# Optimization experiments

Measured on AMD Instinct MI355X. Metric: run time of the kernel, lower is better.

## Reference

```python
import jax, jax.numpy as jnp
import numpy as np

IC, IND, MID, OC, OD, ITERS = 8, 16, 32, 8, 16, 3
B, H, W = 8, 64, 64


def squash(x, axis):
    sq = jnp.sum(x * x, axis=axis, keepdims=True)
    return sq / (0.5 + sq) * x / (jnp.sqrt(sq + 1e-6) + 1e-6)


def gconv(x, w, b, pad):
    # grouped conv over the IC capsule groups (equivalent to the per-capsule
    # Conv2d blocks applied to slices of the capsule axis)
    y = jax.lax.conv_general_dilated(
        x, w, (1, 1), pad,
        dimension_numbers=("NCHW", "OIHW", "NCHW"),
        feature_group_count=IC)
    return y + b[None, :, None, None]


def setup_inputs() -> dict:
    key = jax.random.key(0)
    ks = jax.random.split(key, 7)
    x = jax.random.normal(ks[0], (B, IC * IND, H, W), jnp.float32)
    w1 = jax.random.normal(ks[1], (IC * MID, IND, 1, 1), jnp.float32) * 0.1
    b1 = jax.random.normal(ks[2], (IC * MID,), jnp.float32) * 0.1
    w2 = jax.random.normal(ks[3], (IC * MID, MID, 3, 3), jnp.float32) * 0.05
    b2 = jax.random.normal(ks[4], (IC * MID,), jnp.float32) * 0.1
    w3 = jax.random.normal(ks[5], (IC * OC * OD, MID, 1, 1), jnp.float32) * 0.05
    b3 = jax.random.normal(ks[6], (IC * OC * OD,), jnp.float32) * 0.1
    attn_w = jnp.zeros((1, OC, 1, 1, 1), jnp.float32)  # torch init: zeros
    attn_b = jnp.ones((1, OC, 1, 1, 1), jnp.float32)   # torch init: ones
    return dict(x=x, w1=w1, b1=b1, w2=w2, b2=b2, w3=w3, b3=b3,
                attn_w=attn_w, attn_b=attn_b)


def reference(x, w1, b1, w2, b2, w3, b3, attn_w, attn_b):
    bsz = x.shape[0]
    h_, w_ = x.shape[-2], x.shape[-1]
    # per-capsule conv stack: ReLU -> 1x1 -> ReLU -> 3x3 -> ReLU -> 1x1
    h = jax.nn.relu(x)
    h = jax.nn.relu(gconv(h, w1, b1, "VALID"))
    h = jax.nn.relu(gconv(h, w2, b2, "SAME"))
    h = gconv(h, w3, b3, "VALID")                     # [B, IC*OC*OD, H, W]
    u_hat = h.reshape(bsz, IC, OC, OD, h_, w_)
    u_sq = squash(u_hat, axis=3)
    # dynamic routing
    b = jnp.zeros((bsz, IC, OC, h_, w_), u_hat.dtype)
    for _ in range(ITERS - 1):
        c = jax.nn.sigmoid(b)
        s = jnp.sum(u_sq * c[:, :, :, None], axis=1)   # [B, OC, OD, H, W]
        v = squash(s, axis=2)
        b = b + jnp.sum(u_sq * v[:, None], axis=3)     # [B, IC, OC, H, W]
    c = jax.nn.sigmoid(b)
    s = jnp.sum(u_hat * c[:, :, :, None], axis=1)      # [B, OC, OD, H, W]
    # SpatialCapsuleAttn
    mean_hw = jnp.mean(s, axis=(-2, -1), keepdims=True)        # adaptive avg pool(1)
    avg = jnp.sum(s * mean_hw, axis=2)                         # [B, OC, H, W]
    t = avg.reshape(bsz, OC, h_ * w_)
    m = jnp.mean(t, axis=-1, keepdims=True)
    sd = jnp.std(t, axis=-1, keepdims=True, ddof=1) + 1e-6     # torch std: unbiased
    t = (t - m) / sd
    t = t.reshape(bsz, OC, 1, h_, w_) * attn_w + attn_b
    s = s * jax.nn.sigmoid(t)
    out = s.reshape(bsz, OC * OD, h_, w_) + x
    return out
```

## Files before the change

### kernel.cpp

```cpp
#include <hip/hip_runtime.h>
#include <hip/hip_bf16.h>
#include <hip/hip_fp16.h>

#define HW 4096

typedef _Float16 f16x8 __attribute__((ext_vector_type(8)));
typedef float f32x4 __attribute__((ext_vector_type(4)));

#define FOR8(X) X(0) X(1) X(2) X(3) X(4) X(5) X(6) X(7)

static __device__ __forceinline__ __half2 u2h(unsigned int u) {
    union { unsigned int u; __half2 h; } c; c.u = u; return c.h;
}
static __device__ __forceinline__ unsigned int h2u(__half2 h) {
    union { unsigned int u; __half2 h; } c; c.h = h; return c.u;
}

__global__ __launch_bounds__(256) void k0_prep(const float* __restrict__ w3, ushort* __restrict__ w3h,
                                               const float* __restrict__ w2, ushort* __restrict__ w2f,
                                               float* __restrict__ stats) {
    int bid = blockIdx.x;
    int t = threadIdx.x;
    if (bid == 0 && t < 128) stats[t] = 0.f;
    if (bid < 128) {
        int gi = bid * 256 + t;
        int j = gi & 7;
        int l = (gi >> 3) & 63;
        int p = gi >> 9;
        int ic = p >> 3, oc = p & 7;
        int od = l & 15;
        int m  = ((l >> 4) << 3) + j;
        w3h[gi] = __half_as_ushort(__float2half(w3[(size_t)((ic * 128 + oc * 16 + od) * 32 + m)]));
    } else {
        int gi = (bid - 128) * 256 + t;
        if (gi >= 73728) return;
        int j   = gi & 7;
        int l   = (gi >> 3) & 63;
        int h   = (gi >> 9) & 1;
        int tap = (gi >> 10) % 9;
        int g   = gi / 9216;
        int co = h * 16 + (l & 15);
        int ci = ((l >> 4) << 3) + j;
        w2f[gi] = __half_as_ushort(__float2half(w2[(size_t)((g * 32 + co) * 32 + ci) * 9 + tap]));
    }
}

__global__ __launch_bounds__(256) void k12_conv(const float* __restrict__ x, const float* __restrict__ w1,
                                                const float* __restrict__ b1, const ushort* __restrict__ w2f,
                                                const float* __restrict__ b2, ushort* __restrict__ h2g) {
    __shared__ ushort h1s[6][66][40];

    int bi = blockIdx.x;
    int q  = bi & 15;
    int g  = (bi >> 4) & 7;
    int b  = bi >> 7;
    int y0 = q * 4;
    int t  = threadIdx.x;

    for (int i = t; i < 396; i += 256) {
        int r  = i / 66;
        int xi = i - r * 66;
        int yy = y0 + r - 1;
        int xx = xi - 1;
        bool valid = (yy >= 0) && (yy < 64) && (xx >= 0) && (xx < 64);
        ushort hv[32];
        if (valid) {
            const float* xb = x + (size_t)(b * 128 + g * 16) * HW + yy * 64 + xx;
            float xv[16];
#pragma unroll
            for (int i2 = 0; i2 < 16; ++i2) xv[i2] = fmaxf(xb[i2 * HW], 0.f);
            const float* wg = w1 + g * 512;
            const float* bg = b1 + g * 32;
#pragma unroll
            for (int m = 0; m < 32; ++m) {
                float acc = bg[m];
#pragma unroll
                for (int i2 = 0; i2 < 16; ++i2) acc = fmaf(xv[i2], wg[m * 16 + i2], acc);
                hv[m] = __half_as_ushort(__float2half(fmaxf(acc, 0.f)));
            }
        } else {
#pragma unroll
            for (int m = 0; m < 32; ++m) hv[m] = 0;
        }
        ushort* dst = &h1s[r][xi][0];
#pragma unroll
        for (int q2 = 0; q2 < 4; ++q2) *(uint4*)&dst[q2 * 8] = *(uint4*)&hv[q2 * 8];
    }
    __syncthreads();

    int w  = t >> 6, l = t & 63;
    int lrow = l & 15, kgrp = l >> 4;
    int yloc = w;
    const ushort* wg2 = w2f + (size_t)g * 9216;

    float4 bias0 = *(const float4*)(b2 + g * 32 + kgrp * 4);
    float4 bias1 = *(const float4*)(b2 + g * 32 + 16 + kgrp * 4);

#pragma unroll
    for (int tile = 0; tile < 4; ++tile) {
        int xcol = tile * 16 + lrow;
        f32x4 acc0, acc1;
        acc0[0] = bias0.x; acc0[1] = bias0.y; acc0[2] = bias0.z; acc0[3] = bias0.w;
        acc1[0] = bias1.x; acc1[1] = bias1.y; acc1[2] = bias1.z; acc1[3] = bias1.w;
#pragma unroll
        for (int tap = 0; tap < 9; ++tap) {
            int dy = tap / 3, dx = tap - dy * 3;
            f16x8 Bf = *(const f16x8*)&h1s[yloc + dy][xcol + dx][kgrp * 8];
            f16x8 A0 = *(const f16x8*)&wg2[((tap * 2 + 0) * 64 + l) * 8];
            f16x8 A1 = *(const f16x8*)&wg2[((tap * 2 + 1) * 64 + l) * 8];
            acc0 = __builtin_amdgcn_mfma_f32_16x16x32_f16(A0, Bf, acc0, 0, 0, 0);
            acc1 = __builtin_amdgcn_mfma_f32_16x16x32_f16(A1, Bf, acc1, 0, 0, 0);
        }
        int px = (y0 + yloc) * 64 + xcol;
        ushort* ob = h2g + ((size_t)(b * 8 + g) * HW + px) * 32;
        uint2 wv0, wv1;
        wv0.x = h2u(__floats2half2_rn(fmaxf(acc0[0], 0.f), fmaxf(acc0[1], 0.f)));
        wv0.y = h2u(__floats2half2_rn(fmaxf(acc0[2], 0.f), fmaxf(acc0[3], 0.f)));
        wv1.x = h2u(__floats2half2_rn(fmaxf(acc1[0], 0.f), fmaxf(acc1[1], 0.f)));
        wv1.y = h2u(__floats2half2_rn(fmaxf(acc1[2], 0.f), fmaxf(acc1[3], 0.f)));
        *(uint2*)&ob[kgrp * 4] = wv0;
        *(uint2*)&ob[16 + kgrp * 4] = wv1;
    }
}

__global__ __launch_bounds__(512) void k3f_route(const ushort* __restrict__ h2g, const ushort* __restrict__ w3h,
                                                 const float* __restrict__ b3, ushort* __restrict__ sOut,
                                                 float* __restrict__ part) {
    __shared__ ushort us[32 * 1024];
    __shared__ float wred[8][16][8];
    int bid = blockIdx.x;
    int b   = bid >> 7;
    int px0 = (bid & 127) << 5;
    int t   = threadIdx.x;
    int w   = t >> 6, l = t & 63;

    {
        int ic = w;
        int lrow = l & 15, lk = l >> 4;
        f16x8 bf0 = *(const f16x8*)&h2g[(((size_t)(b * 8 + ic)) * HW + px0 + lrow) * 32 + lk * 8];
        f16x8 bf1 = *(const f16x8*)&h2g[(((size_t)(b * 8 + ic)) * HW + px0 + 16 + lrow) * 32 + lk * 8];
        int s0sw = (lrow & 15) << 3;
#pragma unroll
        for (int oc = 0; oc < 8; ++oc) {
            f16x8 af = *(const f16x8*)&w3h[((ic * 8 + oc) * 64 + l) * 8];
            float4 bv = *(const float4*)(b3 + ic * 128 + oc * 16 + lk * 4);
            f32x4 c0; c0[0] = bv.x; c0[1] = bv.y; c0[2] = bv.z; c0[3] = bv.w;
            int ch = ic * 128 + oc * 16 + lk * 4;
            f32x4 d0 = __builtin_amdgcn_mfma_f32_16x16x32_f16(af, bf0, c0, 0, 0, 0);
            uint2 wv0;
            wv0.x = h2u(__floats2half2_rn(d0[0], d0[1]));
            wv0.y = h2u(__floats2half2_rn(d0[2], d0[3]));
            *(uint2*)&us[lrow * 1024 + (ch ^ s0sw)] = wv0;
            f32x4 d1 = __builtin_amdgcn_mfma_f32_16x16x32_f16(af, bf1, c0, 0, 0, 0);
            uint2 wv1;
            wv1.x = h2u(__floats2half2_rn(d1[0], d1[1]));
            wv1.y = h2u(__floats2half2_rn(d1[2], d1[3]));
            *(uint2*)&us[(16 + lrow) * 1024 + (ch ^ s0sw)] = wv1;
        }
    }
    __syncthreads();

    int px  = t >> 4;
    int oc  = (t >> 1) & 7;
    int odh = t & 1;
    int ssw = (px & 15) << 3;
    const ushort* ur = &us[px * 1024];
#define LDQ(i) uint4 q##i = *(const uint4*)&ur[((i) * 128 + oc * 16 + odh * 8) ^ ssw];
    FOR8(LDQ)
#undef LDQ
    __syncthreads();

#define UNP(i) float2 f0 = __half22float2(u2h(q##i.x)), f1 = __half22float2(u2h(q##i.y)), \
                      f2 = __half22float2(u2h(q##i.z)), f3 = __half22float2(u2h(q##i.w));

#define SC(i) float sc##i; { UNP(i) \
        float sp = f0.x*f0.x + f0.y*f0.y + f1.x*f1.x + f1.y*f1.y \
                 + f2.x*f2.x + f2.y*f2.y + f3.x*f3.x + f3.y*f3.y; \
        sp += __shfl_xor(sp, 1); \
        sc##i = sp / ((0.5f + sp) * (sqrtf(sp + 1e-6f) + 1e-6f)); }
    FOR8(SC)
#undef SC

#define BRI(i) float br##i = 0.f;
    FOR8(BRI)
#undef BRI

    float s0, s1, s2, s3, s4, s5, s6, s7;
#pragma unroll
    for (int it = 0; it < 2; ++it) {
#define CSC(i) float cs##i = sc##i / (1.f + __expf(-br##i));
        FOR8(CSC)
#undef CSC
        s0 = s1 = s2 = s3 = s4 = s5 = s6 = s7 = 0.f;
#define SVA(i) { UNP(i) \
        s0 = fmaf(f0.x, cs##i, s0); s1 = fmaf(f0.y, cs##i, s1); \
        s2 = fmaf(f1.x, cs##i, s2); s3 = fmaf(f1.y, cs##i, s3); \
        s4 = fmaf(f2.x, cs##i, s4); s5 = fmaf(f2.y, cs##i, s5); \
        s6 = fmaf(f3.x, cs##i, s6); s7 = fmaf(f3.y, cs##i, s7); }
        FOR8(SVA)
#undef SVA
        float sp = s0*s0 + s1*s1 + s2*s2 + s3*s3 + s4*s4 + s5*s5 + s6*s6 + s7*s7;
        sp += __shfl_xor(sp, 1);
        float f = sp / ((0.5f + sp) * (sqrtf(sp + 1e-6f) + 1e-6f));
#define DOTD(i) { UNP(i) \
        float dp = f0.x*s0 + f0.y*s1 + f1.x*s2 + f1.y*s3 + f2.x*s4 + f2.y*s5 + f3.x*s6 + f3.y*s7; \
        dp += __shfl_xor(dp, 1); \
        br##i = fmaf(sc##i * f, dp, br##i); }
        FOR8(DOTD)
#undef DOTD
    }

#define CF(i) float cf##i = 1.f / (1.f + __expf(-br##i));
    FOR8(CF)
#undef CF
    s0 = s1 = s2 = s3 = s4 = s5 = s6 = s7 = 0.f;
#define FS(i) { UNP(i) \
        s0 = fmaf(f0.x, cf##i, s0); s1 = fmaf(f0.y, cf##i, s1); \
        s2 = fmaf(f1.x, cf##i, s2); s3 = fmaf(f1.y, cf##i, s3); \
        s4 = fmaf(f2.x, cf##i, s4); s5 = fmaf(f2.y, cf##i, s5); \
        s6 = fmaf(f3.x, cf##i, s6); s7 = fmaf(f3.y, cf##i, s7); }
    FOR8(FS)
#undef FS
#undef UNP

    {
        uint4 pk;
        pk.x = h2u(__floats2half2_rn(s0, s1));
        pk.y = h2u(__floats2half2_rn(s2, s3));
        pk.z = h2u(__floats2half2_rn(s4, s5));
        pk.w = h2u(__floats2half2_rn(s6, s7));
        *(uint4*)&us[px * 1024 + ((oc * 16 + odh * 8) ^ ssw)] = pk;
    }

    {
        float p0 = s0, p1 = s1, p2 = s2, p3 = s3, p4 = s4, p5 = s5, p6 = s6, p7 = s7;
#pragma unroll
        for (int m = 16; m <= 32; m <<= 1) {
            p0 += __shfl_xor(p0, m); p1 += __shfl_xor(p1, m);
            p2 += __shfl_xor(p2, m); p3 += __shfl_xor(p3, m);
            p4 += __shfl_xor(p4, m); p5 += __shfl_xor(p5, m);
            p6 += __shfl_xor(p6, m); p7 += __shfl_xor(p7, m);
        }
        if ((l & 48) == 0) {
            float* wr = wred[w][oc * 2 + odh];
            wr[0] = p0; wr[1] = p1; wr[2] = p2; wr[3] = p3;
            wr[4] = p4; wr[5] = p5; wr[6] = p6; wr[7] = p7;
        }
    }
    __syncthreads();

    {
        int oc2 = w;
        int pxw = l >> 1, half = l & 1;
        int ch2 = (oc2 * 16 + half * 8) ^ ((pxw & 15) << 3);
        uint4 v = *(const uint4*)&us[pxw * 1024 + ch2];
        ushort* sb = sOut + ((size_t)(b * 8 + oc2) * 4096 + px0 + pxw) * 16 + half * 8;
        *(uint4*)sb = v;
    }
    if (t < 128) {
        int comb = t >> 3, j = t & 7;
        float a = 0.f;
#pragma unroll
        for (int ww = 0; ww < 8; ++ww) a += wred[ww][comb][j];
        int oc3 = comb >> 1, odh3 = comb & 1;
        part[((size_t)(b * 8 + oc3) * 128 + (bid & 127)) * 16 + odh3 * 8 + j] = a;
    }
}

__global__ __launch_bounds__(256) void k4_avg(const ushort* __restrict__ sIn, const float* __restrict__ part,
                                              float* __restrict__ avg, float* __restrict__ stats) {
    __shared__ float mh[16];
    int bi = blockIdx.x;
    int chunk = bi & 15;
    int bo = bi >> 4;
    int t = threadIdx.x;
    int pos = chunk * 256 + t;

    if (t < 16) {
        float a = 0.f;
        for (int c = 0; c < 128; ++c) a += part[(size_t)(bo * 128 + c) * 16 + t];
        mh[t] = a * (1.f / 4096.f);
    }
    __syncthreads();

    const ushort* sb = sIn + ((size_t)bo * 4096 + pos) * 16;
    uint4 qa = *(const uint4*)&sb[0];
    uint4 qb = *(const uint4*)&sb[8];
    float2 f0 = __half22float2(u2h(qa.x)), f1 = __half22float2(u2h(qa.y));
    float2 f2 = __half22float2(u2h(qa.z)), f3 = __half22float2(u2h(qa.w));
    float2 f4 = __half22float2(u2h(qb.x)), f5 = __half22float2(u2h(qb.y));
    float2 f6 = __half22float2(u2h(qb.z)), f7 = __half22float2(u2h(qb.w));
    float a = f0.x * mh[0] + f0.y * mh[1] + f1.x * mh[2] + f1.y * mh[3]
            + f2.x * mh[4] + f2.y * mh[5] + f3.x * mh[6] + f3.y * mh[7]
            + f4.x * mh[8] + f4.y * mh[9] + f5.x * mh[10] + f5.y * mh[11]
            + f6.x * mh[12] + f6.y * mh[13] + f7.x * mh[14] + f7.y * mh[15];
    avg[(size_t)bo * 4096 + pos] = a;

    float p1 = a, p2 = a * a;
#pragma unroll
    for (int m = 1; m < 64; m <<= 1) {
        p1 += __shfl_xor(p1, m);
        p2 += __shfl_xor(p2, m);
    }
    if ((t & 63) == 0) {
        atomicAdd(&stats[bo * 2],     p1);
        atomicAdd(&stats[bo * 2 + 1], p2);
    }
}

__global__ __launch_bounds__(256) void k5_out(const ushort* __restrict__ sIn, const float* __restrict__ x,
                                              const float* __restrict__ avg, const float* __restrict__ stats,
                                              const float* __restrict__ aw, const float* __restrict__ ab,
                                              float* __restrict__ out) {
    int bi = blockIdx.x;
    int chunk = bi & 15;
    int bo = bi >> 4;
    int oc = bo & 7;
    int pos = chunk * 256 + threadIdx.x;

    float sum = stats[bo * 2], sumsq = stats[bo * 2 + 1];
    float m   = sum * (1.f / 4096.f);
    float var = (sumsq - 4096.f * m * m) * (1.f / 4095.f);
    float sd  = sqrtf(fmaxf(var, 0.f)) + 1e-6f;

    float t   = (avg[(size_t)bo * 4096 + pos] - m) / sd * aw[oc] + ab[oc];
    float sig = 1.f / (1.f + __expf(-t));

    const ushort* sb = sIn + ((size_t)bo * 4096 + pos) * 16;
    uint4 qa = *(const uint4*)&sb[0];
    uint4 qb = *(const uint4*)&sb[8];
    float2 f0 = __half22float2(u2h(qa.x)), f1 = __half22float2(u2h(qa.y));
    float2 f2 = __half22float2(u2h(qa.z)), f3 = __half22float2(u2h(qa.w));
    float2 f4 = __half22float2(u2h(qb.x)), f5 = __half22float2(u2h(qb.y));
    float2 f6 = __half22float2(u2h(qb.z)), f7 = __half22float2(u2h(qb.w));
    float sv[16] = {f0.x, f0.y, f1.x, f1.y, f2.x, f2.y, f3.x, f3.y,
                    f4.x, f4.y, f5.x, f5.y, f6.x, f6.y, f7.x, f7.y};

    const float* xb = x + (size_t)bo * 16 * HW + pos;
    float* ob = out + (size_t)bo * 16 * HW + pos;
#pragma unroll
    for (int od = 0; od < 16; ++od) ob[od * HW] = fmaf(sv[od], sig, xb[od * HW]);
}

extern "C" void kernel_launch(void* const* d_in, const int* in_sizes, int n_in,
                              void* d_out, int out_size, void* d_ws, size_t ws_size,
                              hipStream_t stream) {
    const float* x  = (const float*)d_in[0];
    const float* w1 = (const float*)d_in[1];
    const float* b1 = (const float*)d_in[2];
    const float* w2 = (const float*)d_in[3];
    const float* b2 = (const float*)d_in[4];
    const float* w3 = (const float*)d_in[5];
    const float* b3 = (const float*)d_in[6];
    const float* aw = (const float*)d_in[7];
    const float* ab = (const float*)d_in[8];

    float* ws      = (float*)d_ws;
    ushort* h2g    = (ushort*)ws;
    ushort* sbuf   = (ushort*)(ws + 4194304);
    float* avg     = ws + 4194304 + 2097152;
    float* part    = avg + 262144;
    float* stats   = part + 131072;
    ushort* w3h    = (ushort*)(stats + 128);
    ushort* w2f    = w3h + 32768;

    k0_prep  <<<416, 256, 0, stream>>>(w3, w3h, w2, w2f, stats);
    k12_conv <<<1024, 256, 0, stream>>>(x, w1, b1, w2f, b2, h2g);
    k3f_route<<<1024, 512, 0, stream>>>(h2g, w3h, b3, sbuf, part);
    k4_avg   <<<1024, 256, 0, stream>>>(sbuf, part, avg, stats);
    k5_out   <<<1024, 256, 0, stream>>>(sbuf, x, avg, stats, aw, ab, (float*)d_out);
}
```

Before: 85.63 us.

## Use packed fp16 math in routing and recompute attention avg in output kernel

The routing loop in k3f_route now runs its squash norms, weighted sums and agreement dot products with packed half2 FMAs instead of unpacking to fp32. The goal is to cut VALU work and register pressure. Separately, k4 no longer writes the per-pixel avg array; it stores only the 16 mean values, and k5 recomputes the avg dot product from the s data it already loads. This drops a global write and a read of 1 MB. The risk is lower numerical precision, since accumulation happens in fp16, and possible overflow of squared sums.

```diff
diff --git a/kernel.cpp b/kernel.cpp
--- a/kernel.cpp
+++ b/kernel.cpp
@@ -170,12 +170,12 @@
 #undef LDQ
     __syncthreads();
 
-#define UNP(i) float2 f0 = __half22float2(u2h(q##i.x)), f1 = __half22float2(u2h(q##i.y)), \
-                      f2 = __half22float2(u2h(q##i.z)), f3 = __half22float2(u2h(q##i.w));
-
-#define SC(i) float sc##i; { UNP(i) \
-        float sp = f0.x*f0.x + f0.y*f0.y + f1.x*f1.x + f1.y*f1.y \
-                 + f2.x*f2.x + f2.y*f2.y + f3.x*f3.x + f3.y*f3.y; \
+#define SC(i) float sc##i; { \
+        __half2 a0 = u2h(q##i.x), a1 = u2h(q##i.y), a2 = u2h(q##i.z), a3 = u2h(q##i.w); \
+        __half2 s2 = __hmul2(a0, a0); s2 = __hfma2(a1, a1, s2); \
+        s2 = __hfma2(a2, a2, s2); s2 = __hfma2(a3, a3, s2); \
+        float2 fq = __half22float2(s2); \
+        float sp = fq.x + fq.y; \
         sp += __shfl_xor(sp, 1); \
         sc##i = sp / ((0.5f + sp) * (sqrtf(sp + 1e-6f) + 1e-6f)); }
     FOR8(SC)
@@ -185,55 +185,52 @@
     FOR8(BRI)
 #undef BRI
 
-    float s0, s1, s2, s3, s4, s5, s6, s7;
+    __half2 sh0, sh1, sh2, sh3;
 #pragma unroll
     for (int it = 0; it < 2; ++it) {
-#define CSC(i) float cs##i = sc##i / (1.f + __expf(-br##i));
+#define CSC(i) __half2 cs##i = __float2half2_rn(sc##i / (1.f + __expf(-br##i)));
         FOR8(CSC)
 #undef CSC
-        s0 = s1 = s2 = s3 = s4 = s5 = s6 = s7 = 0.f;
-#define SVA(i) { UNP(i) \
-        s0 = fmaf(f0.x, cs##i, s0); s1 = fmaf(f0.y, cs##i, s1); \
-        s2 = fmaf(f1.x, cs##i, s2); s3 = fmaf(f1.y, cs##i, s3); \
-        s4 = fmaf(f2.x, cs##i, s4); s5 = fmaf(f2.y, cs##i, s5); \
-        s6 = fmaf(f3.x, cs##i, s6); s7 = fmaf(f3.y, cs##i, s7); }
+        sh0 = sh1 = sh2 = sh3 = __float2half2_rn(0.f);
+#define SVA(i) { sh0 = __hfma2(u2h(q##i.x), cs##i, sh0); sh1 = __hfma2(u2h(q##i.y), cs##i, sh1); \
+                 sh2 = __hfma2(u2h(q##i.z), cs##i, sh2); sh3 = __hfma2(u2h(q##i.w), cs##i, sh3); }
         FOR8(SVA)
 #undef SVA
-        float sp = s0*s0 + s1*s1 + s2*s2 + s3*s3 + s4*s4 + s5*s5 + s6*s6 + s7*s7;
+        __half2 n2 = __hmul2(sh0, sh0); n2 = __hfma2(sh1, sh1, n2);
+        n2 = __hfma2(sh2, sh2, n2); n2 = __hfma2(sh3, sh3, n2);
+        float2 nf = __half22float2(n2);
+        float sp = nf.x + nf.y;
         sp += __shfl_xor(sp, 1);
-        float f = sp / ((0.5f + sp) * (sqrtf(sp + 1e-6f) + 1e-6f));
-#define DOTD(i) { UNP(i) \
-        float dp = f0.x*s0 + f0.y*s1 + f1.x*s2 + f1.y*s3 + f2.x*s4 + f2.y*s5 + f3.x*s6 + f3.y*s7; \
+        float fsq = sp / ((0.5f + sp) * (sqrtf(sp + 1e-6f) + 1e-6f));
+#define DOTD(i) { __half2 d2 = __hmul2(u2h(q##i.x), sh0); d2 = __hfma2(u2h(q##i.y), sh1, d2); \
+        d2 = __hfma2(u2h(q##i.z), sh2, d2); d2 = __hfma2(u2h(q##i.w), sh3, d2); \
+        float2 df = __half22float2(d2); float dp = df.x + df.y; \
         dp += __shfl_xor(dp, 1); \
-        br##i = fmaf(sc##i * f, dp, br##i); }
+        br##i = fmaf(sc##i * fsq, dp, br##i); }
         FOR8(DOTD)
 #undef DOTD
     }
 
-#define CF(i) float cf##i = 1.f / (1.f + __expf(-br##i));
+#define CF(i) __half2 cf##i = __float2half2_rn(1.f / (1.f + __expf(-br##i)));
     FOR8(CF)
 #undef CF
-    s0 = s1 = s2 = s3 = s4 = s5 = s6 = s7 = 0.f;
-#define FS(i) { UNP(i) \
-        s0 = fmaf(f0.x, cf##i, s0); s1 = fmaf(f0.y, cf##i, s1); \
-        s2 = fmaf(f1.x, cf##i, s2); s3 = fmaf(f1.y, cf##i, s3); \
-        s4 = fmaf(f2.x, cf##i, s4); s5 = fmaf(f2.y, cf##i, s5); \
-        s6 = fmaf(f3.x, cf##i, s6); s7 = fmaf(f3.y, cf##i, s7); }
+    sh0 = sh1 = sh2 = sh3 = __float2half2_rn(0.f);
+#define FS(i) { sh0 = __hfma2(u2h(q##i.x), cf##i, sh0); sh1 = __hfma2(u2h(q##i.y), cf##i, sh1); \
+                sh2 = __hfma2(u2h(q##i.z), cf##i, sh2); sh3 = __hfma2(u2h(q##i.w), cf##i, sh3); }
     FOR8(FS)
 #undef FS
-#undef UNP
 
     {
         uint4 pk;
-        pk.x = h2u(__floats2half2_rn(s0, s1));
-        pk.y = h2u(__floats2half2_rn(s2, s3));
-        pk.z = h2u(__floats2half2_rn(s4, s5));
-        pk.w = h2u(__floats2half2_rn(s6, s7));
+        pk.x = h2u(sh0); pk.y = h2u(sh1); pk.z = h2u(sh2); pk.w = h2u(sh3);
         *(uint4*)&us[px * 1024 + ((oc * 16 + odh * 8) ^ ssw)] = pk;
     }
 
     {
-        float p0 = s0, p1 = s1, p2 = s2, p3 = s3, p4 = s4, p5 = s5, p6 = s6, p7 = s7;
+        float2 g0 = __half22float2(sh0), g1 = __half22float2(sh1);
+        float2 g2 = __half22float2(sh2), g3 = __half22float2(sh3);
+        float p0 = g0.x, p1 = g0.y, p2 = g1.x, p3 = g1.y;
+        float p4 = g2.x, p5 = g2.y, p6 = g3.x, p7 = g3.y;
 #pragma unroll
         for (int m = 16; m <= 32; m <<= 1) {
             p0 += __shfl_xor(p0, m); p1 += __shfl_xor(p1, m);
@@ -267,8 +264,8 @@
     }
 }
 
-__global__ __launch_bounds__(256) void k4_avg(const ushort* __restrict__ sIn, const float* __restrict__ part,
-                                              float* __restrict__ avg, float* __restrict__ stats) {
+__global__ __launch_bounds__(256) void k4_stats(const ushort* __restrict__ sIn, const float* __restrict__ part,
+                                                float* __restrict__ mhOut, float* __restrict__ stats) {
     __shared__ float mh[16];
     int bi = blockIdx.x;
     int chunk = bi & 15;
@@ -279,7 +276,9 @@
     if (t < 16) {
         float a = 0.f;
         for (int c = 0; c < 128; ++c) a += part[(size_t)(bo * 128 + c) * 16 + t];
-        mh[t] = a * (1.f / 4096.f);
+        float v = a * (1.f / 4096.f);
+        mh[t] = v;
+        if (chunk == 0) mhOut[bo * 16 + t] = v;
     }
     __syncthreads();
 
@@ -294,7 +293,6 @@
             + f2.x * mh[4] + f2.y * mh[5] + f3.x * mh[6] + f3.y * mh[7]
             + f4.x * mh[8] + f4.y * mh[9] + f5.x * mh[10] + f5.y * mh[11]
             + f6.x * mh[12] + f6.y * mh[13] + f7.x * mh[14] + f7.y * mh[15];
-    avg[(size_t)bo * 4096 + pos] = a;
 
     float p1 = a, p2 = a * a;
 #pragma unroll
@@ -309,22 +307,24 @@
 }
 
 __global__ __launch_bounds__(256) void k5_out(const ushort* __restrict__ sIn, const float* __restrict__ x,
-                                              const float* __restrict__ avg, const float* __restrict__ stats,
+                                              const float* __restrict__ mhIn, const float* __restrict__ stats,
                                               const float* __restrict__ aw, const float* __restrict__ ab,
                                               float* __restrict__ out) {
+    __shared__ float mh[16];
     int bi = blockIdx.x;
     int chunk = bi & 15;
     int bo = bi >> 4;
     int oc = bo & 7;
-    int pos = chunk * 256 + threadIdx.x;
+    int t = threadIdx.x;
+    int pos = chunk * 256 + t;
+
+    if (t < 16) mh[t] = mhIn[bo * 16 + t];
+    __syncthreads();
 
     float sum = stats[bo * 2], sumsq = stats[bo * 2 + 1];
     float m   = sum * (1.f / 4096.f);
     float var = (sumsq - 4096.f * m * m) * (1.f / 4095.f);
     float sd  = sqrtf(fmaxf(var, 0.f)) + 1e-6f;
-
-    float t   = (avg[(size_t)bo * 4096 + pos] - m) / sd * aw[oc] + ab[oc];
-    float sig = 1.f / (1.f + __expf(-t));
 
     const ushort* sb = sIn + ((size_t)bo * 4096 + pos) * 16;
     uint4 qa = *(const uint4*)&sb[0];
@@ -335,6 +335,13 @@
     float2 f6 = __half22float2(u2h(qb.z)), f7 = __half22float2(u2h(qb.w));
     float sv[16] = {f0.x, f0.y, f1.x, f1.y, f2.x, f2.y, f3.x, f3.y,
                     f4.x, f4.y, f5.x, f5.y, f6.x, f6.y, f7.x, f7.y};
+
+    float a = 0.f;
+#pragma unroll
+    for (int od = 0; od < 16; ++od) a = fmaf(sv[od], mh[od], a);
+
+    float tt  = (a - m) / sd * aw[oc] + ab[oc];
+    float sig = 1.f / (1.f + __expf(-tt));
 
     const float* xb = x + (size_t)bo * 16 * HW + pos;
     float* ob = out + (size_t)bo * 16 * HW + pos;
@@ -358,15 +365,15 @@
     float* ws      = (float*)d_ws;
     ushort* h2g    = (ushort*)ws;
     ushort* sbuf   = (ushort*)(ws + 4194304);
-    float* avg     = ws + 4194304 + 2097152;
-    float* part    = avg + 262144;
+    float* part    = ws + 4194304 + 2097152;
     float* stats   = part + 131072;
-    ushort* w3h    = (ushort*)(stats + 128);
+    float* mhBuf   = stats + 128;
+    ushort* w3h    = (ushort*)(mhBuf + 1024);
     ushort* w2f    = w3h + 32768;
 
     k0_prep  <<<416, 256, 0, stream>>>(w3, w3h, w2, w2f, stats);
     k12_conv <<<1024, 256, 0, stream>>>(x, w1, b1, w2f, b2, h2g);
     k3f_route<<<1024, 512, 0, stream>>>(h2g, w3h, b3, sbuf, part);
-    k4_avg   <<<1024, 256, 0, stream>>>(sbuf, part, avg, stats);
-    k5_out   <<<1024, 256, 0, stream>>>(sbuf, x, avg, stats, aw, ab, (float*)d_out);
-}
+    k4_stats <<<1024, 256, 0, stream>>>(sbuf, part, mhBuf, stats);
+    k5_out   <<<1024, 256, 0, stream>>>(sbuf, x, mhBuf, stats, aw, ab, (float*)d_out);
+}
```

Result: no change. 84.76 us (-1.0%).
